# Optimization experiments

Measured on AMD Instinct MI355X. Metric: run time of the kernel, lower is better.

Reference implementation:

```python
import jax, jax.numpy as jnp
import numpy as np

K = 7        # kernel_size
OUT = 10     # out_channels
CIN = 1      # in_channels
IH = 306     # input spatial size (square)
POOL = 10    # max_pool1d kernel/stride


def setup_inputs() -> dict:
    key = jax.random.key(0)
    k1, k2, k3 = jax.random.split(key, 3)
    stdv = 1.0 / np.sqrt(CIN * K * K)  # matches reset_parameters()
    x = jax.random.normal(k1, (1, CIN, IH, IH), dtype=jnp.float32)
    K_hit = jax.random.uniform(k2, (OUT, CIN, K, K), dtype=jnp.float32, minval=-stdv, maxval=stdv)
    K_miss = jax.random.uniform(k3, (OUT, CIN, K, K), dtype=jnp.float32, minval=-stdv, maxval=stdv)
    return {"input": x, "K_hit": K_hit, "K_miss": K_miss}


def _patches(x, k):
    # Sliding windows, stride 1, valid padding: (B, C, k, k, fh, fw).
    B, C, H, W = x.shape
    fh, fw = H - k + 1, W - k + 1
    rows = []
    for u in range(k):          # fixed small loop over kernel rows
        cols = [x[:, :, u:u + fh, v:v + fw] for v in range(k)]
        rows.append(jnp.stack(cols, axis=2))   # (B, C, k, fh, fw)
    return jnp.stack(rows, axis=2)             # (B, C, k, k, fh, fw)


def reference(input, K_hit, K_miss):
    B, cin, ih, _ = input.shape
    out, k = K_hit.shape[0], K_hit.shape[2]
    fh = ih - k + 1
    out_fmap = cin * out

    p = _patches(input, k)                                # (B, cin, k, k, fh, fh)
    p = p[:, None]                                        # (B, 1, cin, k, k, fh, fh)
    kh = K_hit[None, :, :, :, :, None, None]              # (1, out, cin, k, k, 1, 1)
    km = K_miss[None, :, :, :, :, None, None]

    # -relu(-(x - K_hit)) == min(x - K_hit, 0); summed over ALL windows + kernel taps -> (B, out)
    F_hit_sum = jnp.sum(jnp.minimum(p - kh, 0.0), axis=(2, 3, 4, 5, 6))
    F_miss_sum = jnp.sum(jnp.maximum(p - km, 0.0), axis=(2, 3, 4, 5, 6))
    F_map_val = F_hit_sum - F_miss_sum                    # (B, out)

    def expand(v):  # broadcast (B, out) scalar-per-channel over (cin*fh*fh), view as feature map
        return jnp.broadcast_to(v[:, :, None], (B, out, cin * fh * fh)).reshape(B, out_fmap, fh, fh)

    F_map = expand(F_map_val)
    F_hit_list = expand(F_hit_sum)
    F_miss_list = expand(F_miss_sum)

    # torch.squeeze then F.max_pool1d(kernel=10): pool over the last spatial axis.
    sq = jnp.squeeze(F_map)                               # (out_fmap, fh, fh) since B=1
    L = sq.shape[-1]
    nwin = L // POOL
    pooled = sq[..., : nwin * POOL].reshape(sq.shape[:-1] + (nwin, POOL)).max(-1)

    return pooled, F_hit_list, F_miss_list
```

## Files before the change

kernel.cpp:

```cpp
#include <hip/hip_runtime.h>

#define IHH 306
#define KW 7
#define OUTC 10
#define FH 300
#define NPIX (FH * FH)
#define KK (KW * KW)
#define BLK 512
#define GRID 176
#define PPB 512
#define NROWS 21
#define OUT4 472500
#define POOLED_END 90000
#define HIT_END 990000
#define CHUNK4 2685


#define AL(p)    __hip_atomic_load((p), __ATOMIC_RELAXED, __HIP_MEMORY_SCOPE_AGENT)
#define AS(p, v) __hip_atomic_store((p), (v), __ATOMIC_RELAXED, __HIP_MEMORY_SCOPE_AGENT)

__global__ __launch_bounds__(BLK) void k_fused(
    const float* __restrict__ x,
    const float* __restrict__ kh,
    const float* __restrict__ km,
    float* __restrict__ partials,
    int* __restrict__ done,
    float* __restrict__ pub,
    int* __restrict__ ready,
    float4* __restrict__ out)
{
    __shared__ float2 s_k[KK * OUTC];
    __shared__ float s_red[BLK / 64][NROWS];
    __shared__ float s_part[NROWS][16];
    __shared__ float s_ks[2 * OUTC];
    __shared__ float s_o[3 * OUTC];

    const int t = threadIdx.x;
    const int b = blockIdx.x;

    for (int i = t; i < KK * OUTC; i += BLK) {
        const int tap = i / OUTC;
        const int o = i - tap * OUTC;
        s_k[i] = make_float2(kh[o * KK + tap], km[o * KK + tap]);
    }
    __syncthreads();

    float ah[OUTC], am[OUTC];
    float sx = 0.0f;
#pragma unroll
    for (int o = 0; o < OUTC; ++o) { ah[o] = 0.0f; am[o] = 0.0f; }

    const int p = b * PPB + t;
    if (p < NPIX) {
        const int i = p / FH;
        const int j = p - i * FH;
        const float* xr = x + i * IHH + j;
        for (int u = 0; u < KW; ++u) {
            for (int v = 0; v < KW; ++v) {
                const float xv = xr[u * IHH + v];
                sx += xv;
                const float2* wk = &s_k[(u * KW + v) * OUTC];
#pragma unroll
                for (int o = 0; o < OUTC; ++o) {
                    const float2 w = wk[o];
                    ah[o] += fabsf(xv - w.x);
                    am[o] += fabsf(xv - w.y);
                }
            }
        }
    }

    const int lane = t & 63;
    const int wave = t >> 6;
    float vals[NROWS];
#pragma unroll
    for (int o = 0; o < OUTC; ++o) { vals[o] = ah[o]; vals[OUTC + o] = am[o]; }
    vals[2 * OUTC] = sx;
#pragma unroll
    for (int r = 0; r < NROWS; ++r) {
        float v = vals[r];
#pragma unroll
        for (int s = 32; s > 0; s >>= 1) v += __shfl_xor(v, s);
        if (lane == 0) s_red[wave][r] = v;
    }
    __syncthreads();
    if (t < NROWS) {
        float s = 0.0f;
#pragma unroll
        for (int w = 0; w < BLK / 64; ++w) s += s_red[w][t];
        AS(&partials[t * GRID + b], s);
    }
    __syncthreads();
    if (t == 0) AS(&done[b * 16], 1);

    if (b == 0) {
        if (t >= 336 && t < 336 + 2 * OUTC) {
            const int a = t - 336;
            const float* kp = (a < OUTC) ? (kh + a * KK)
                                         : (km + (a - OUTC) * KK);
            float s = 0.0f;
            for (int q = 0; q < KK; ++q) s += kp[q];
            s_ks[a] = s;
        }
        if (t < GRID) {
            while (AL(&done[t * 16]) == 0) __builtin_amdgcn_s_sleep(2);
        }
        __syncthreads();

        if (t < NROWS * 16) {
            const int r = t >> 4;
            const int s16 = t & 15;
            float acc = 0.0f;
            for (int c = s16; c < GRID; c += 16)
                acc += AL(&partials[r * GRID + c]);
            s_part[r][s16] = acc;
        }
        __syncthreads();
        if (t < NROWS) {
            float f = 0.0f;
#pragma unroll
            for (int s = 0; s < 16; ++s) f += s_part[t][s];
            s_part[t][0] = f;
        }
        __syncthreads();
        if (t < OUTC) {
            const float Sx = s_part[2 * OUTC][0];
            const float Ah = s_part[t][0];
            const float Am = s_part[OUTC + t][0];
            const float Fh = 0.5f * ((Sx - (float)NPIX * s_ks[t]) - Ah);
            const float Fm = 0.5f * ((Sx - (float)NPIX * s_ks[OUTC + t]) + Am);
            s_o[t] = Fh - Fm;
            s_o[OUTC + t] = Fh;
            s_o[2 * OUTC + t] = Fm;
            AS(&pub[t], Fh - Fm);
            AS(&pub[OUTC + t], Fh);
            AS(&pub[2 * OUTC + t], Fm);
        }
        __syncthreads();
        if (t == 0) AS(ready, 1);
        __syncthreads();
    } else {
        if (t == 0) {
            while (AL(ready) == 0) __builtin_amdgcn_s_sleep(8);
        }
        __syncthreads();
        if (t < 3 * OUTC) s_o[t] = AL(&pub[t]);
        __syncthreads();
    }

    const int start = b * CHUNK4;
    const int stop = min(start + CHUNK4, OUT4);
    for (int i4 = start + t; i4 < stop; i4 += BLK) {
        const int base = i4 * 4;
        float v;
        if (base < POOLED_END) {
            v = s_o[base / 9000];
        } else if (base < HIT_END) {
            v = s_o[OUTC + (base - POOLED_END) / 90000];
        } else {
            v = s_o[2 * OUTC + (base - HIT_END) / 90000];
        }
        out[i4] = make_float4(v, v, v, v);
    }
}

extern "C" void kernel_launch(void* const* d_in, const int* in_sizes, int n_in,
                              void* d_out, int out_size, void* d_ws, size_t ws_size,
                              hipStream_t stream) {
    const float* x  = (const float*)d_in[0];
    const float* kh = (const float*)d_in[1];
    const float* km = (const float*)d_in[2];
    float4* out = (float4*)d_out;

    float* partials = (float*)d_ws;
    int*   done     = (int*)((char*)d_ws + 16384);
    float* pub      = (float*)((char*)d_ws + 27648);
    int*   ready    = (int*)((char*)d_ws + 27776);

    (void)hipMemsetAsync((char*)d_ws + 16384, 0, 12288, stream);
    k_fused<<<GRID, BLK, 0, stream>>>(x, kh, km, partials, done, pub, ready, out);
}
```

Measured before the change: 33.76 us.

## Have every block reduce partials itself instead of waiting on block zero

Every block now polls all done flags, reduces the 176×21 partials redundantly and computes the final channel values locally. This removes the second grid-wide handoff, where block zero published results and raised a ready flag that other blocks polled. The done flags are now packed contiguously rather than one per 64 bytes, the memset covers only 176 ints, and the kernel-tap sums are taken from shared memory. The cost is redundant reduction work and heavier polling of the flags by every block, plus possible contention from packed flags sharing cache lines.

```diff
diff --git a/kernel.cpp b/kernel.cpp
--- a/kernel.cpp
+++ b/kernel.cpp
@@ -8,7 +8,6 @@
 #define KK (KW * KW)
 #define BLK 512
 #define GRID 176
-#define PPB 512
 #define NROWS 21
 #define OUT4 472500
 #define POOLED_END 90000
@@ -25,8 +24,6 @@
     const float* __restrict__ km,
     float* __restrict__ partials,
     int* __restrict__ done,
-    float* __restrict__ pub,
-    int* __restrict__ ready,
     float4* __restrict__ out)
 {
     __shared__ float2 s_k[KK * OUTC];
@@ -50,7 +47,7 @@
 #pragma unroll
     for (int o = 0; o < OUTC; ++o) { ah[o] = 0.0f; am[o] = 0.0f; }
 
-    const int p = b * PPB + t;
+    const int p = b * BLK + t;
     if (p < NPIX) {
         const int i = p / FH;
         const int j = p - i * FH;
@@ -91,62 +88,51 @@
         AS(&partials[t * GRID + b], s);
     }
     __syncthreads();
-    if (t == 0) AS(&done[b * 16], 1);
+    if (t == 0) AS(&done[b], 1);
 
-    if (b == 0) {
-        if (t >= 336 && t < 336 + 2 * OUTC) {
-            const int a = t - 336;
-            const float* kp = (a < OUTC) ? (kh + a * KK)
-                                         : (km + (a - OUTC) * KK);
-            float s = 0.0f;
-            for (int q = 0; q < KK; ++q) s += kp[q];
-            s_ks[a] = s;
+    if (t >= 448 && t < 448 + 2 * OUTC) {
+        const int a = t - 448;
+        const int o = (a < OUTC) ? a : a - OUTC;
+        float s = 0.0f;
+        for (int tap = 0; tap < KK; ++tap) {
+            const float2 w = s_k[tap * OUTC + o];
+            s += (a < OUTC) ? w.x : w.y;
         }
-        if (t < GRID) {
-            while (AL(&done[t * 16]) == 0) __builtin_amdgcn_s_sleep(2);
-        }
-        __syncthreads();
+        s_ks[a] = s;
+    }
 
-        if (t < NROWS * 16) {
-            const int r = t >> 4;
-            const int s16 = t & 15;
-            float acc = 0.0f;
-            for (int c = s16; c < GRID; c += 16)
-                acc += AL(&partials[r * GRID + c]);
-            s_part[r][s16] = acc;
-        }
-        __syncthreads();
-        if (t < NROWS) {
-            float f = 0.0f;
+    if (t < GRID) {
+        while (AL(&done[t]) == 0) __builtin_amdgcn_s_sleep(1);
+    }
+    __syncthreads();
+
+    if (t < NROWS * 16) {
+        const int r = t >> 4;
+        const int s16 = t & 15;
+        float acc = 0.0f;
+        for (int c = s16; c < GRID; c += 16)
+            acc += AL(&partials[r * GRID + c]);
+        s_part[r][s16] = acc;
+    }
+    __syncthreads();
+    if (t < NROWS) {
+        float f = 0.0f;
 #pragma unroll
-            for (int s = 0; s < 16; ++s) f += s_part[t][s];
-            s_part[t][0] = f;
-        }
-        __syncthreads();
-        if (t < OUTC) {
-            const float Sx = s_part[2 * OUTC][0];
-            const float Ah = s_part[t][0];
-            const float Am = s_part[OUTC + t][0];
-            const float Fh = 0.5f * ((Sx - (float)NPIX * s_ks[t]) - Ah);
-            const float Fm = 0.5f * ((Sx - (float)NPIX * s_ks[OUTC + t]) + Am);
-            s_o[t] = Fh - Fm;
-            s_o[OUTC + t] = Fh;
-            s_o[2 * OUTC + t] = Fm;
-            AS(&pub[t], Fh - Fm);
-            AS(&pub[OUTC + t], Fh);
-            AS(&pub[2 * OUTC + t], Fm);
-        }
-        __syncthreads();
-        if (t == 0) AS(ready, 1);
-        __syncthreads();
-    } else {
-        if (t == 0) {
-            while (AL(ready) == 0) __builtin_amdgcn_s_sleep(8);
-        }
-        __syncthreads();
-        if (t < 3 * OUTC) s_o[t] = AL(&pub[t]);
-        __syncthreads();
+        for (int s = 0; s < 16; ++s) f += s_part[t][s];
+        s_part[t][0] = f;
     }
+    __syncthreads();
+    if (t < OUTC) {
+        const float Sx = s_part[2 * OUTC][0];
+        const float Ah = s_part[t][0];
+        const float Am = s_part[OUTC + t][0];
+        const float Fh = 0.5f * ((Sx - (float)NPIX * s_ks[t]) - Ah);
+        const float Fm = 0.5f * ((Sx - (float)NPIX * s_ks[OUTC + t]) + Am);
+        s_o[t] = Fh - Fm;
+        s_o[OUTC + t] = Fh;
+        s_o[2 * OUTC + t] = Fm;
+    }
+    __syncthreads();
 
     const int start = b * CHUNK4;
     const int stop = min(start + CHUNK4, OUT4);
@@ -174,9 +160,7 @@
 
     float* partials = (float*)d_ws;
     int*   done     = (int*)((char*)d_ws + 16384);
-    float* pub      = (float*)((char*)d_ws + 27648);
-    int*   ready    = (int*)((char*)d_ws + 27776);
 
-    (void)hipMemsetAsync((char*)d_ws + 16384, 0, 12288, stream);
-    k_fused<<<GRID, BLK, 0, stream>>>(x, kh, km, partials, done, pub, ready, out);
+    (void)hipMemsetAsync(done, 0, GRID * sizeof(int), stream);
+    k_fused<<<GRID, BLK, 0, stream>>>(x, kh, km, partials, done, out);
 }
```

New measurement: 35.39 us. +4.8%, slower.
